# Kernel optimization log

Measured on AMD Instinct MI355X. Metric: run time of the kernel, lower is better.

Reference implementation:

```python
import jax, jax.numpy as jnp
import numpy as np

N_SAMPLES = 4194304
N_RAYS = 131072


def setup_inputs() -> dict:
    key = jax.random.key(0)
    k1, k2, k3, k4, k5, k6 = jax.random.split(key, 6)
    alpha = jax.random.uniform(k1, (N_SAMPLES, 1), dtype=jnp.float32)
    values3d = jax.random.uniform(k2, (N_SAMPLES, 3), dtype=jnp.float32)
    values1d = jax.random.uniform(k3, (N_SAMPLES, 1), dtype=jnp.float32)
    weights = jax.random.uniform(k4, (N_SAMPLES, 1), dtype=jnp.float32)
    sample_values = jax.random.normal(k5, (N_SAMPLES, 3), dtype=jnp.float32)
    ray_id = jnp.sort(jax.random.randint(k6, (N_SAMPLES,), 0, N_RAYS, dtype=jnp.int32))
    return {"alpha": alpha, "values3d": values3d, "values1d": values1d,
            "weights": weights, "sample_values": sample_values,
            "ray_id": ray_id, "n_rays": N_RAYS}


def _transmittance(alpha, ray_id, n_rays):
    # exclusive cumprod of (1 - alpha) within each packed ray segment, in log space
    logs = jnp.log(jnp.clip(1.0 - alpha[:, 0], 1e-7, 1.0))          # [N]
    csum = jnp.cumsum(logs)
    excl = csum - logs                                               # exclusive cumsum
    first = jnp.concatenate([jnp.ones((1,), bool), ray_id[1:] != ray_id[:-1]])
    seg_base = jax.ops.segment_sum(jnp.where(first, excl, 0.0), ray_id,
                                   num_segments=n_rays)              # [R]
    transmittance = jnp.exp(excl - seg_base[ray_id])[:, None]        # [N,1]
    bg_transmittance = jnp.exp(jax.ops.segment_sum(logs, ray_id,
                                                   num_segments=n_rays))  # [R]
    return transmittance, bg_transmittance


def reference(alpha, values3d, values1d, weights, sample_values, ray_id, n_rays):
    transmittance, bg_transmittance = _transmittance(alpha, ray_id, n_rays)
    # integrate_3d / integrate_1d: per-ray sum of value * weight
    integrated_3d = jax.ops.segment_sum(values3d * weights, ray_id, num_segments=n_rays)  # [R,3]
    integrated_1d = jax.ops.segment_sum(values1d * weights, ray_id, num_segments=n_rays)  # [R,1]
    # SumOverRay: per-ray sum plus broadcast back to each sample
    sum_per_ray = jax.ops.segment_sum(sample_values, ray_id, num_segments=n_rays)         # [R,3]
    sum_per_sample = sum_per_ray[ray_id]                                                  # [N,3]
    return (transmittance, bg_transmittance, integrated_3d, integrated_1d,
            sum_per_ray, sum_per_sample)
```

## Files before the change

kernel.cpp:

```cpp
#include <hip/hip_runtime.h>

typedef float f32x4 __attribute__((ext_vector_type(4)));

template<int CTRL>
__device__ __forceinline__ float dpp1(float x) {
    return __int_as_float(__builtin_amdgcn_update_dpp(
        0x3f800000, __float_as_int(x), CTRL, 0xF, 0xF, false));
}
template<int CTRL>
__device__ __forceinline__ float dpp0(float x) {
    return __int_as_float(__builtin_amdgcn_update_dpp(
        0, __float_as_int(x), CTRL, 0xF, 0xF, true));
}
template<int PAT>
__device__ __forceinline__ float swz(float x) {
    return __int_as_float(__builtin_amdgcn_ds_swizzle(__float_as_int(x), PAT));
}
#define FUNNEL16(v) do { \
    v += dpp0<0x111>(v); \
    v += dpp0<0x112>(v); \
    v += dpp0<0x114>(v); \
    v += dpp0<0x118>(v); } while (0)
#define BFLY16(v) do { \
    v += swz<0x041F>(v); \
    v += swz<0x081F>(v); \
    v += swz<0x101F>(v); \
    v += swz<0x201F>(v); } while (0)

__device__ __forceinline__ void ntst4(float* p, float x, float y, float z, float w) {
    f32x4 v = {x, y, z, w};
    __builtin_nontemporal_store(v, (f32x4*)p);
}

__global__ __launch_bounds__(256) void seg_bounds_kernel(
    const int* __restrict__ ray_id, int n, int* __restrict__ seg_se)
{
    int i = blockIdx.x * blockDim.x + threadIdx.x;
    if (i >= n) return;
    int rid = ray_id[i];
    if (i == 0 || ray_id[i - 1] != rid) seg_se[2 * rid + 0] = i;
    if (i == n - 1 || ray_id[i + 1] != rid) seg_se[2 * rid + 1] = i + 1;
}

__global__ __launch_bounds__(256) void ray_kernel(
    const float* __restrict__ alpha,
    const float* __restrict__ values3d,
    const float* __restrict__ values1d,
    const float* __restrict__ weights,
    const float* __restrict__ sample_values,
    const int*   __restrict__ seg_se,
    float* __restrict__ out_T,
    float* __restrict__ out_bg,
    float* __restrict__ out_i3,
    float* __restrict__ out_i1,
    float* __restrict__ out_spr,
    float* __restrict__ out_sps,
    int R)
{
    const int lane = threadIdx.x & 63;
    const int wid  = threadIdx.x >> 6;
    const int j    = lane & 15;
    const int g    = lane >> 4;
    const int r    = (blockIdx.x * 4 + wid) * 4 + g;
    const bool ray_ok = (r < R);
    const int rc = ray_ok ? r : 0;

    const int2 se = ((const int2*)seg_se)[rc];
    int s0 = se.x, s1 = se.y;
    if (!ray_ok) { s0 = 0; s1 = 0; }

    float c = 1.0f;
    float i3x = 0.f, i3y = 0.f, i3z = 0.f, i1 = 0.f;
    float sx = 0.f, sy = 0.f, sz = 0.f;

    const int base0 = s0 & ~3;

    for (int base = base0; base < s1; base += 64) {
        const int a = base + 4 * j;
        const bool tile_ok = (a < s1);
        const int  al = tile_ok ? a : base0;

        const f32x4 av  = *(const f32x4*)(alpha + al);
        const f32x4 wv  = *(const f32x4*)(weights + al);
        const f32x4 v1v = *(const f32x4*)(values1d + al);
        const f32x4 b0  = *(const f32x4*)(values3d + 3 * al);
        const f32x4 b1  = *(const f32x4*)(values3d + 3 * al + 4);
        const f32x4 b2  = *(const f32x4*)(values3d + 3 * al + 8);
        const f32x4 q0  = *(const f32x4*)(sample_values + 3 * al);
        const f32x4 q1  = *(const f32x4*)(sample_values + 3 * al + 4);
        const f32x4 q2  = *(const f32x4*)(sample_values + 3 * al + 8);

        const bool w0 = tile_ok & (a + 0 >= s0);
        const bool w1 = tile_ok & (a + 1 >= s0) & (a + 1 < s1);
        const bool w2 = tile_ok & (a + 2 >= s0) & (a + 2 < s1);
        const bool w3 = tile_ok & (a + 3 < s1);

        float o0 = fminf(fmaxf(1.0f - av.x, 1e-7f), 1.0f); if (!w0) o0 = 1.0f;
        float o1 = fminf(fmaxf(1.0f - av.y, 1e-7f), 1.0f); if (!w1) o1 = 1.0f;
        float o2 = fminf(fmaxf(1.0f - av.z, 1e-7f), 1.0f); if (!w2) o2 = 1.0f;
        float o3 = fminf(fmaxf(1.0f - av.w, 1e-7f), 1.0f); if (!w3) o3 = 1.0f;

        const float p01  = o0 * o1;
        const float p012 = p01 * o2;
        float p = p012 * o3;

        p *= dpp1<0x111>(p);
        p *= dpp1<0x112>(p);
        p *= dpp1<0x114>(p);
        p *= dpp1<0x118>(p);
        const float gincl = p;
        const float gexcl = dpp1<0x111>(gincl);

        const float cg = c * gexcl;
        const float t0 = cg;
        const float t1 = cg * o0;
        const float t2 = cg * p01;
        const float t3 = cg * p012;

        const float W0 = w0 ? wv.x : 0.f;
        const float W1 = w1 ? wv.y : 0.f;
        const float W2 = w2 ? wv.z : 0.f;
        const float W3 = w3 ? wv.w : 0.f;
        const float M0 = w0 ? 1.f : 0.f;
        const float M1 = w1 ? 1.f : 0.f;
        const float M2 = w2 ? 1.f : 0.f;
        const float M3 = w3 ? 1.f : 0.f;

        i1  += v1v.x * W0 + v1v.y * W1 + v1v.z * W2 + v1v.w * W3;
        i3x += b0.x * W0 + b0.w * W1 + b1.z * W2 + b2.y * W3;
        i3y += b0.y * W0 + b1.x * W1 + b1.w * W2 + b2.z * W3;
        i3z += b0.z * W0 + b1.y * W1 + b2.x * W2 + b2.w * W3;
        sx  += q0.x * M0 + q0.w * M1 + q1.z * M2 + q2.y * M3;
        sy  += q0.y * M0 + q1.x * M1 + q1.w * M2 + q2.z * M3;
        sz  += q0.z * M0 + q1.y * M1 + q2.x * M2 + q2.w * M3;

        if (w0 & w1 & w2 & w3) {
            ntst4(out_T + a, t0, t1, t2, t3);
        } else {
            if (w0) out_T[a + 0] = t0;
            if (w1) out_T[a + 1] = t1;
            if (w2) out_T[a + 2] = t2;
            if (w3) out_T[a + 3] = t3;
        }

        c *= swz<0x1F0>(gincl);
    }

    FUNNEL16(i3x); FUNNEL16(i3y); FUNNEL16(i3z); FUNNEL16(i1);
    BFLY16(sx);  BFLY16(sy);  BFLY16(sz);

    if (ray_ok && j == 15) {
        out_bg[r] = c;
        out_i3[3 * r + 0] = i3x;
        out_i3[3 * r + 1] = i3y;
        out_i3[3 * r + 2] = i3z;
        out_i1[r] = i1;
        out_spr[3 * r + 0] = sx;
        out_spr[3 * r + 1] = sy;
        out_spr[3 * r + 2] = sz;
    }

    for (int base = base0; base < s1; base += 64) {
        const int a = base + 4 * j;
        const bool tile_ok = (a < s1);
        const bool w0 = tile_ok & (a + 0 >= s0);
        const bool w1 = tile_ok & (a + 1 >= s0) & (a + 1 < s1);
        const bool w2 = tile_ok & (a + 2 >= s0) & (a + 2 < s1);
        const bool w3 = tile_ok & (a + 3 < s1);
        if (w0 & w1 & w2 & w3) {
            ntst4(out_sps + 3 * a,     sx, sy, sz, sx);
            ntst4(out_sps + 3 * a + 4, sy, sz, sx, sy);
            ntst4(out_sps + 3 * a + 8, sz, sx, sy, sz);
        } else {
            if (w0) { out_sps[3*a+0] = sx; out_sps[3*a+1]  = sy; out_sps[3*a+2]  = sz; }
            if (w1) { out_sps[3*a+3] = sx; out_sps[3*a+4]  = sy; out_sps[3*a+5]  = sz; }
            if (w2) { out_sps[3*a+6] = sx; out_sps[3*a+7]  = sy; out_sps[3*a+8]  = sz; }
            if (w3) { out_sps[3*a+9] = sx; out_sps[3*a+10] = sy; out_sps[3*a+11] = sz; }
        }
    }
}

extern "C" void kernel_launch(void* const* d_in, const int* in_sizes, int n_in,
                              void* d_out, int out_size, void* d_ws, size_t ws_size,
                              hipStream_t stream) {
    const float* alpha = (const float*)d_in[0];
    const float* v3    = (const float*)d_in[1];
    const float* v1    = (const float*)d_in[2];
    const float* w     = (const float*)d_in[3];
    const float* sv    = (const float*)d_in[4];
    const int*   rid   = (const int*)d_in[5];

    int N = in_sizes[0];
    int R = (out_size - 4 * N) / 8;

    int* seg_se = (int*)d_ws;
    (void)hipMemsetAsync(d_ws, 0, (size_t)2 * R * sizeof(int), stream);

    float* out     = (float*)d_out;
    float* out_T   = out;
    float* out_bg  = out + N;
    float* out_i3  = out_bg + R;
    float* out_i1  = out_i3 + 3 * (size_t)R;
    float* out_spr = out_i1 + R;
    float* out_sps = out_spr + 3 * (size_t)R;

    seg_bounds_kernel<<<(N + 255) / 256, 256, 0, stream>>>(rid, N, seg_se);

    int blocks = (R + 15) / 16;
    ray_kernel<<<blocks, 256, 0, stream>>>(alpha, v3, v1, w, sv, seg_se,
                                           out_T, out_bg, out_i3, out_i1, out_spr,
                                           out_sps, R);
}
```

Baseline: 55.76 us.

## Drop workspace memset, vectorize segment bounds, validate segments in ray kernel

```diff
diff --git a/kernel.cpp b/kernel.cpp
--- a/kernel.cpp
+++ b/kernel.cpp
@@ -21,11 +21,6 @@
     v += dpp0<0x112>(v); \
     v += dpp0<0x114>(v); \
     v += dpp0<0x118>(v); } while (0)
-#define BFLY16(v) do { \
-    v += swz<0x041F>(v); \
-    v += swz<0x081F>(v); \
-    v += swz<0x101F>(v); \
-    v += swz<0x201F>(v); } while (0)
 
 __device__ __forceinline__ void ntst4(float* p, float x, float y, float z, float w) {
     f32x4 v = {x, y, z, w};
@@ -35,11 +30,18 @@
 __global__ __launch_bounds__(256) void seg_bounds_kernel(
     const int* __restrict__ ray_id, int n, int* __restrict__ seg_se)
 {
-    int i = blockIdx.x * blockDim.x + threadIdx.x;
-    if (i >= n) return;
-    int rid = ray_id[i];
-    if (i == 0 || ray_id[i - 1] != rid) seg_se[2 * rid + 0] = i;
-    if (i == n - 1 || ray_id[i + 1] != rid) seg_se[2 * rid + 1] = i + 1;
+    const int t = blockIdx.x * blockDim.x + threadIdx.x;
+    const int a = t * 4;
+    if (a >= n) return;
+    const int4 rv = *(const int4*)(ray_id + a);
+    const int prev = (a == 0) ? -1 : ray_id[a - 1];
+    const int nxt  = (a + 4 < n) ? ray_id[a + 4] : -1;
+
+    if (rv.x != prev) seg_se[2 * rv.x] = a;
+    if (rv.y != rv.x) { seg_se[2 * rv.x + 1] = a + 1; seg_se[2 * rv.y] = a + 1; }
+    if (rv.z != rv.y) { seg_se[2 * rv.y + 1] = a + 2; seg_se[2 * rv.z] = a + 2; }
+    if (rv.w != rv.z) { seg_se[2 * rv.z + 1] = a + 3; seg_se[2 * rv.w] = a + 3; }
+    if (rv.w != nxt)  seg_se[2 * rv.w + 1] = a + 4;
 }
 
 __global__ __launch_bounds__(256) void ray_kernel(
@@ -48,6 +50,7 @@
     const float* __restrict__ values1d,
     const float* __restrict__ weights,
     const float* __restrict__ sample_values,
+    const int*   __restrict__ ray_id,
     const int*   __restrict__ seg_se,
     float* __restrict__ out_T,
     float* __restrict__ out_bg,
@@ -55,7 +58,7 @@
     float* __restrict__ out_i1,
     float* __restrict__ out_spr,
     float* __restrict__ out_sps,
-    int R)
+    int R, int N)
 {
     const int lane = threadIdx.x & 63;
     const int wid  = threadIdx.x >> 6;
@@ -67,7 +70,9 @@
 
     const int2 se = ((const int2*)seg_se)[rc];
     int s0 = se.x, s1 = se.y;
-    if (!ray_ok) { s0 = 0; s1 = 0; }
+    bool valid = ray_ok & (s0 >= 0) & (s0 < s1) & (s1 <= N);
+    if (valid) valid = (ray_id[s0] == rc);
+    if (!valid) { s0 = 0; s1 = 0; }
 
     float c = 1.0f;
     float i3x = 0.f, i3y = 0.f, i3z = 0.f, i1 = 0.f;
@@ -147,7 +152,10 @@
     }
 
     FUNNEL16(i3x); FUNNEL16(i3y); FUNNEL16(i3z); FUNNEL16(i1);
-    BFLY16(sx);  BFLY16(sy);  BFLY16(sz);
+    FUNNEL16(sx);  FUNNEL16(sy);  FUNNEL16(sz);
+    sx = swz<0x1F0>(sx);
+    sy = swz<0x1F0>(sy);
+    sz = swz<0x1F0>(sz);
 
     if (ray_ok && j == 15) {
         out_bg[r] = c;
@@ -194,7 +202,6 @@
     int R = (out_size - 4 * N) / 8;
 
     int* seg_se = (int*)d_ws;
-    (void)hipMemsetAsync(d_ws, 0, (size_t)2 * R * sizeof(int), stream);
 
     float* out     = (float*)d_out;
     float* out_T   = out;
@@ -204,10 +211,11 @@
     float* out_spr = out_i1 + R;
     float* out_sps = out_spr + 3 * (size_t)R;
 
-    seg_bounds_kernel<<<(N + 255) / 256, 256, 0, stream>>>(rid, N, seg_se);
+    const int nquad = N / 4;
+    seg_bounds_kernel<<<(nquad + 255) / 256, 256, 0, stream>>>(rid, N, seg_se);
 
     int blocks = (R + 15) / 16;
-    ray_kernel<<<blocks, 256, 0, stream>>>(alpha, v3, v1, w, sv, seg_se,
+    ray_kernel<<<blocks, 256, 0, stream>>>(alpha, v3, v1, w, sv, rid, seg_se,
                                            out_T, out_bg, out_i3, out_i1, out_spr,
-                                           out_sps, R);
-}
+                                           out_sps, R, N);
+}
```

Result: faster. 50.00 us (-10.3%).
